# Optimization experiments

Measured on AMD Instinct MI355X. Metric: run time of the kernel, lower is better.

The kernel has to match this reference:

```python
import jax, jax.numpy as jnp
import numpy as np

N_QUBITS = 12
N_LAYERS = 4
BATCH = 4096
DIM = 2 ** N_QUBITS


def _ry(t):
    # t: (B,) real -> (B,2,2) complex64 ; RY = [[c,-s],[s,c]], c=cos(t/2), s=sin(t/2)
    c = jnp.cos(t / 2).astype(jnp.complex64)
    s = jnp.sin(t / 2).astype(jnp.complex64)
    return jnp.stack([jnp.stack([c, -s], -1), jnp.stack([s, c], -1)], -2)


def _rx(t):
    # RX = [[c,-i s],[-i s,c]]
    c = jnp.cos(t / 2).astype(jnp.complex64)
    s = (-1j) * jnp.sin(t / 2).astype(jnp.complex64)
    return jnp.stack([jnp.stack([c, s], -1), jnp.stack([s, c], -1)], -2)


def _rz(t):
    # RZ = diag(e^{-i t/2}, e^{+i t/2})
    e = jnp.exp(-0.5j * t.astype(jnp.complex64))
    z = jnp.zeros_like(e)
    return jnp.stack([jnp.stack([e, z], -1), jnp.stack([z, jnp.conj(e)], -1)], -2)


def _apply1(state, q, mat):
    # state: (B, 2^n) complex; mat: (B,2,2); qubit q is the q-th most significant bit
    B = state.shape[0]
    s = state.reshape(B, 2 ** q, 2, -1)
    return jnp.einsum('bij,bajm->baim', mat, s).reshape(B, DIM)


_CNOT_PERM = np.array([0, 1, 3, 2])  # control=1 -> flip target


def _cnot_adj(state, c):
    # CNOT(control=c, target=c+1), adjacent qubits
    B = state.shape[0]
    s = state.reshape(B, 2 ** c, 4, -1)
    return s[:, :, _CNOT_PERM, :].reshape(B, DIM)


def _parity():
    idx = np.arange(DIM)
    pop = np.zeros(DIM, dtype=np.int64)
    for k in range(N_QUBITS):
        pop += (idx >> k) & 1
    return jnp.asarray(1.0 - 2.0 * (pop % 2), dtype=jnp.float32)


def setup_inputs() -> dict:
    key = jax.random.key(0)
    k1, k2 = jax.random.split(key)
    x = jax.random.uniform(k1, (BATCH,), dtype=jnp.float32)
    thetas = jax.random.normal(k2, (N_LAYERS, N_QUBITS, 3), dtype=jnp.float32)
    return {"x": x, "thetas": thetas}


def reference(x, thetas):
    x = x.ravel()
    B = x.shape[0]
    x1 = jnp.arcsin(x)          # RY feature-map angles
    x2 = jnp.arccos(x ** 2)     # RZ feature-map angles
    state = jnp.zeros((B, DIM), jnp.complex64).at[:, 0].set(1.0)
    ry_fm = _ry(x1)
    rz_fm = _rz(x2)
    for l in range(N_LAYERS):
        for q in range(N_QUBITS):
            state = _apply1(state, q, ry_fm)
        for q in range(N_QUBITS):
            state = _apply1(state, q, rz_fm)
        for q in range(N_QUBITS):
            t = thetas[l, q]
            state = _apply1(state, q, _rx(jnp.broadcast_to(t[0], (B,))))
            state = _apply1(state, q, _rz(jnp.broadcast_to(t[1], (B,))))
            state = _apply1(state, q, _rx(jnp.broadcast_to(t[2], (B,))))
        for j in range(N_QUBITS - 1):
            state = _cnot_adj(state, j)
    abs2 = jnp.real(state) ** 2 + jnp.imag(state) ** 2
    return jnp.einsum('bs,s->b', abs2, _parity())  # <Z0 Z1 ... Z_{n-1}> per batch
```

## Files before the change

### kernel.cpp

```cpp
#include <hip/hip_runtime.h>

namespace {

constexpr int NQ = 12;
constexpr int DIM = 1 << NQ;
constexpr int THREADS = 256;

struct c32 { float r, i; };

__device__ __forceinline__ c32 cmul(c32 a, c32 b) {
    return { fmaf(a.r, b.r, -(a.i * b.i)), fmaf(a.r, b.i, a.i * b.r) };
}

__device__ __forceinline__ void bfy(c32& x, c32& y, float cb, float sb) {
    const c32 a = x, b = y;
    x.r = fmaf(cb, a.r, -(sb * b.r));
    x.i = fmaf(cb, a.i, -(sb * b.i));
    y.r = fmaf(sb, a.r, cb * b.r);
    y.i = fmaf(sb, a.i, cb * b.i);
}

template<int BP>
__device__ __forceinline__ void applyRY(c32 v[16], float cb, float sb) {
    #pragma unroll
    for (int mi = 0; mi < 8; ++mi) {
        const int i0 = ((mi >> BP) << (BP + 1)) | (mi & ((1 << BP) - 1));
        bfy(v[i0], v[i0 | (1 << BP)], cb, sb);
    }
}

__host__ __device__ constexpr int G(int t, int k) {
    for (int i = 0; i < k; ++i) t = (t ^ (t >> 1)) & 0xFFF;
    return t;
}
__host__ __device__ constexpr int Cm(int t) {
    int lo = 0;
    if (t & 0x010) lo ^= 0x2;
    if (t & 0x020) lo ^= 0x4;
    if (t & 0x040) lo ^= 0x8;
    if (t & 0x080) lo ^= 0x6;
    if (t & 0x100) lo ^= 0xA;
    if (t & 0x200) lo ^= 0xC;
    return t ^ lo;
}
__host__ __device__ constexpr int maskE_calc() {
    int m = 0;
    for (int i = 0; i < 12; ++i) {
        int v = G(Cm(1 << i), 12), p = 0;
        while (v) { p ^= (v & 1); v >>= 1; }
        if (p) m |= (1 << i);
    }
    return m;
}
constexpr int MASKE = maskE_calc();

__device__ __forceinline__ void diagTree(c32 T[16], c32 C,
                                         const c32 pf0[4], const c32 pf1[4],
                                         const c32 qv[4], int sigma) {
    const c32 one = { 1.f, 0.f };
    T[0] = C;
    #pragma unroll
    for (int m = 3; m >= 0; --m) {
        const c32 qs0 = sigma ? qv[m] : one;
        const c32 qs1 = sigma ? one : qv[m];
        const c32 g00 = cmul(pf0[m], qs0);
        const c32 g01 = cmul(pf0[m], qs1);
        const c32 g10 = cmul(pf1[m], qs0);
        const c32 g11 = cmul(pf1[m], qs1);
        #pragma unroll
        for (int e = (1 << (3 - m)) - 1; e >= 0; --e) {
            const int j0 = e << (m + 1);
            const int sfxhi = __popc(e) & 1;
            const c32 ga = sfxhi ? g01 : g00;
            const c32 gb = sfxhi ? g10 : g11;
            T[j0 | (1 << m)] = cmul(T[j0], gb);
            T[j0]            = cmul(T[j0], ga);
        }
    }
}

__global__ __launch_bounds__(THREADS)
void qcirc_kernel(const float* __restrict__ x, const float* __restrict__ thetas,
                  float* __restrict__ out) {
    __shared__ alignas(16) float2 amp[DIM];
    __shared__ float4 Vs[4 * NQ * 2];
    __shared__ float2 TbS[2][2][16];
    __shared__ float2 CHiS[2][16];
    __shared__ float2 CLoS[2][2][16];
    __shared__ float red[4];
    float4* a4 = reinterpret_cast<float4*>(amp);

    const int tid = threadIdx.x;
    const int b = blockIdx.x;

    const float xv = x[b];
    const float x1 = asinf(xv);
    const float x2 = acosf(xv * xv);
    const float cy = cosf(0.5f * x1), sy = sinf(0.5f * x1);
    const float cz = cosf(0.5f * x2), sz = sinf(0.5f * x2);
    const c32 M00 = {  cz * cy, -sz * cy };
    const c32 M01 = { -cz * sy,  sz * sy };
    const c32 M10 = {  cz * sy,  sz * sy };
    const c32 M11 = {  cz * cy,  sz * cy };

    if (tid < 4 * NQ) {
        const float* th = thetas + tid * 3;
        const float h0 = 0.5f * th[0], h1 = 0.5f * th[1], h2 = 0.5f * th[2];
        const float c0 = cosf(h0), s0 = sinf(h0);
        const float c1 = cosf(h1), s1 = sinf(h1);
        const float c2 = cosf(h2), s2 = sinf(h2);
        const c32 z0 = { c1, -s1 }, z1 = { c1, s1 };
        const c32 X00 = { c0, 0.f }, X01 = { 0.f, -s0 };
        const c32 A00 = cmul(z0, X00), A01 = cmul(z0, X01);
        const c32 A10 = cmul(z1, X01), A11 = cmul(z1, X00);
        const c32 Y00 = { c2, 0.f }, Y01 = { 0.f, -s2 };
        const c32 U00 = { Y00.r*A00.r - Y00.i*A00.i + Y01.r*A10.r - Y01.i*A10.i,
                          Y00.r*A00.i + Y00.i*A00.r + Y01.r*A10.i + Y01.i*A10.r };
        const c32 U01 = { Y00.r*A01.r - Y00.i*A01.i + Y01.r*A11.r - Y01.i*A11.i,
                          Y00.r*A01.i + Y00.i*A01.r + Y01.r*A11.i + Y01.i*A11.r };
        const c32 U10 = { Y01.r*A00.r - Y01.i*A00.i + Y00.r*A10.r - Y00.i*A10.i,
                          Y01.r*A00.i + Y01.i*A00.r + Y00.r*A10.i + Y00.i*A10.r };
        const c32 U11 = { Y01.r*A01.r - Y01.i*A01.i + Y00.r*A11.r - Y00.i*A11.i,
                          Y01.r*A01.i + Y01.i*A01.r + Y00.r*A11.i + Y00.i*A11.r };
        const c32 V00 = { U00.r*M00.r - U00.i*M00.i + U01.r*M10.r - U01.i*M10.i,
                          U00.r*M00.i + U00.i*M00.r + U01.r*M10.i + U01.i*M10.r };
        const c32 V01 = { U00.r*M01.r - U00.i*M01.i + U01.r*M11.r - U01.i*M11.i,
                          U00.r*M01.i + U00.i*M01.r + U01.r*M11.i + U01.i*M11.r };
        const c32 V10 = { U10.r*M00.r - U10.i*M00.i + U11.r*M10.r - U11.i*M10.i,
                          U10.r*M00.i + U10.i*M00.r + U11.r*M10.i + U11.i*M10.r };
        const c32 V11 = { U10.r*M01.r - U10.i*M01.i + U11.r*M11.r - U11.i*M11.i,
                          U10.r*M01.i + U10.i*M01.r + U11.r*M11.i + U11.i*M11.r };

        float cb = sqrtf(V00.r*V00.r + V00.i*V00.i);
        float sb = sqrtf(V10.r*V10.r + V10.i*V10.i);
        c32 p0, p1, q1;
        const float eps = 1e-6f;
        if (sb <= eps) {
            const float icb = 1.f / cb;
            p0 = { V00.r*icb, V00.i*icb };
            p1 = { V11.r*icb, V11.i*icb };
            q1 = { 1.f, 0.f };
            cb = 1.f; sb = 0.f;
        } else if (cb <= eps) {
            const float isb = 1.f / sb;
            p1 = { V10.r*isb, V10.i*isb };
            p0 = { -V01.r*isb, -V01.i*isb };
            q1 = { 1.f, 0.f };
            cb = 0.f; sb = 1.f;
        } else {
            const float icb = 1.f / cb, isb = 1.f / sb;
            p0 = { V00.r*icb, V00.i*icb };
            p1 = { V10.r*isb, V10.i*isb };
            const c32 t = { V11.r*p1.r + V11.i*p1.i, V11.i*p1.r - V11.r*p1.i };
            q1 = { t.r*icb, t.i*icb };
        }
        Vs[tid * 2]     = make_float4(cb, sb, p0.r, p0.i);
        Vs[tid * 2 + 1] = make_float4(p1.r, p1.i, q1.r, q1.i);
    }
    __syncthreads();

    if (tid < 64) {
        const int bK = (tid >> 5) + 1;
        const int sg = (tid >> 4) & 1;
        const int j  = tid & 15;
        c32 acc = { 1.f, 0.f };
        #pragma unroll
        for (int m = 3; m >= 0; --m) {
            const int Q = 11 - m;
            const float4 s0 = Vs[(bK*NQ+Q)*2];
            const float4 s1 = Vs[(bK*NQ+Q)*2+1];
            const float4 n1 = Vs[((bK+1)*NQ+Q)*2+1];
            const c32 pf = ((j >> m) & 1) ? c32{ s1.x, s1.y } : c32{ s0.z, s0.w };
            acc = cmul(acc, pf);
            if (sg ^ (__popc(j >> m) & 1)) acc = cmul(acc, c32{ n1.z, n1.w });
        }
        TbS[bK-1][sg][j] = make_float2(acc.r, acc.i);
    } else if (tid < 96) {
        const int idx = tid - 64;
        const int bK = (idx >> 4) + 1;
        const int h  = idx & 15;
        c32 acc = { 1.f, 0.f };
        #pragma unroll
        for (int Q = 0; Q < 4; ++Q) {
            const float4 s0 = Vs[(bK*NQ+Q)*2];
            const float4 s1 = Vs[(bK*NQ+Q)*2+1];
            const float4 n1 = Vs[((bK+1)*NQ+Q)*2+1];
            const c32 pf = ((h >> (3-Q)) & 1) ? c32{ s1.x, s1.y } : c32{ s0.z, s0.w };
            acc = cmul(acc, pf);
            if (__popc(h >> (3-Q)) & 1) acc = cmul(acc, c32{ n1.z, n1.w });
        }
        CHiS[bK-1][h] = make_float2(acc.r, acc.i);
    } else if (tid < 160) {
        const int idx = tid - 96;
        const int bK = (idx >> 5) + 1;
        const int sh = (idx >> 4) & 1;
        const int lo = idx & 15;
        c32 acc = { 1.f, 0.f };
        #pragma unroll
        for (int Q = 4; Q < 8; ++Q) {
            const float4 s0 = Vs[(bK*NQ+Q)*2];
            const float4 s1 = Vs[(bK*NQ+Q)*2+1];
            const float4 n1 = Vs[((bK+1)*NQ+Q)*2+1];
            const c32 pf = ((lo >> (7-Q)) & 1) ? c32{ s1.x, s1.y } : c32{ s0.z, s0.w };
            acc = cmul(acc, pf);
            if (sh ^ (__popc(lo >> (7-Q)) & 1)) acc = cmul(acc, c32{ n1.z, n1.w });
        }
        CLoS[bK-1][sh][lo] = make_float2(acc.r, acc.i);
    }

    {
        const int sg0 = __popc(tid) & 1;
        c32 C = { 1.f, 0.f };
        #pragma unroll
        for (int q = 0; q < 8; ++q) {
            const float4 s0 = Vs[q*2];
            const float4 s1 = Vs[q*2+1];
            const bool bit = (tid >> (7 - q)) & 1;
            const c32 e = bit ? c32{ s1.x * s0.y, s1.y * s0.y }
                             : c32{ s0.z * s0.x, s0.w * s0.x };
            C = cmul(C, e);
            const float4 n1 = Vs[(NQ+q)*2+1];
            if (__popc(tid >> (7 - q)) & 1) C = cmul(C, c32{ n1.z, n1.w });
        }
        c32 pf0[4], pf1[4], qv[4];
        #pragma unroll
        for (int m = 0; m < 4; ++m) {
            const int Q = 11 - m;
            const float4 s0 = Vs[Q*2];
            const float4 s1 = Vs[Q*2+1];
            const float4 n1 = Vs[(NQ+Q)*2+1];
            pf0[m] = { s0.z * s0.x, s0.w * s0.x };
            pf1[m] = { s1.x * s0.y, s1.y * s0.y };
            qv[m]  = { n1.z, n1.w };
        }
        c32 T[16];
        diagTree(T, C, pf0, pf1, qv, sg0);
        const int beta = Cm(tid << 4);
        #pragma unroll
        for (int m = 0; m < 8; ++m)
            a4[(beta ^ (2 * m)) >> 1] =
                make_float4(T[2*m].r, T[2*m].i, T[2*m+1].r, T[2*m+1].i);
    }
    __syncthreads();

    const int Lo = tid & 15, Hh = tid >> 4;

    #define RUN_LAYER(K)                                                            \
    {                                                                               \
                                              \
        {                                                                           \
            const float4 g0 = Vs[(K*NQ+0)*2], g1 = Vs[(K*NQ+1)*2];                  \
            const float4 g2 = Vs[(K*NQ+2)*2], g3 = Vs[(K*NQ+3)*2];                  \
            const int beta = Cm(G(tid, K));                                         \
            c32 v[16];                                                              \
            _Pragma("unroll")                                                       \
            for (int j = 0; j < 16; ++j) {                                          \
                const float2 t = amp[beta ^ Cm(G(j << 8, K))];                      \
                v[j] = { t.x, t.y };                                                \
            }                                                                       \
            applyRY<3>(v, g0.x, g0.y); applyRY<2>(v, g1.x, g1.y);                   \
            applyRY<1>(v, g2.x, g2.y); applyRY<0>(v, g3.x, g3.y);                   \
            _Pragma("unroll")                                                       \
            for (int j = 0; j < 16; ++j)                                            \
                amp[beta ^ Cm(G(j << 8, K))] = make_float2(v[j].r, v[j].i);         \
            __syncthreads();                                                        \
        }                                                                           \
                                               \
        {                                                                           \
            const float4 g0 = Vs[(K*NQ+4)*2], g1 = Vs[(K*NQ+5)*2];                  \
            const float4 g2 = Vs[(K*NQ+6)*2], g3 = Vs[(K*NQ+7)*2];                  \
            const int beta = Cm(G((Hh << 8) | Lo, K));                              \
            c32 v[16];                                                              \
            _Pragma("unroll")                                                       \
            for (int j = 0; j < 16; ++j) {                                          \
                const float2 t = amp[beta ^ Cm(G(j << 4, K))];                      \
                v[j] = { t.x, t.y };                                                \
            }                                                                       \
            applyRY<3>(v, g0.x, g0.y); applyRY<2>(v, g1.x, g1.y);                   \
            applyRY<1>(v, g2.x, g2.y); applyRY<0>(v, g3.x, g3.y);                   \
            _Pragma("unroll")                                                       \
            for (int j = 0; j < 16; ++j)                                            \
                amp[beta ^ Cm(G(j << 4, K))] = make_float2(v[j].r, v[j].i);         \
            __syncthreads();                                                        \
        }                                                                           \
            \
        {                                                                           \
            const float4 g0 = Vs[(K*NQ+8)*2],  g1 = Vs[(K*NQ+9)*2];                 \
            const float4 g2 = Vs[(K*NQ+10)*2], g3 = Vs[(K*NQ+11)*2];                \
            const int beta = Cm(G((Hh << 8) | (Lo << 4), K));                       \
            c32 v[16];                                                              \
            _Pragma("unroll")                                                       \
            for (int m = 0; m < 8; ++m) {                                           \
                const int gg = Cm(G(2 * m, K));                                     \
                const float4 F = a4[(beta ^ (gg & ~1)) >> 1];                       \
                const c32 flo = { F.x, F.y }, fhi = { F.z, F.w };                   \
                if (gg & 1) { v[2*m+1] = flo; v[2*m] = fhi; }                       \
                else        { v[2*m] = flo;   v[2*m+1] = fhi; }                     \
            }                                                                       \
            applyRY<3>(v, g0.x, g0.y); applyRY<2>(v, g1.x, g1.y);                   \
            applyRY<1>(v, g2.x, g2.y); applyRY<0>(v, g3.x, g3.y);                   \
            if constexpr (K < 3) {                                                  \
                const int sgm = __popc(tid) & 1;                                    \
                const int sgh = __popc(tid >> 4) & 1;                               \
                const float2 ch = CHiS[K-1][Hh];                                    \
                const float2 cl = CLoS[K-1][sgh][Lo];                               \
                const c32 CT = cmul(c32{ch.x,ch.y}, c32{cl.x,cl.y});                \
                _Pragma("unroll")                                                   \
                for (int j = 0; j < 16; ++j) {                                      \
                    const float2 tb = TbS[K-1][sgm][j];                             \
                    v[j] = cmul(v[j], cmul(CT, c32{tb.x, tb.y}));                   \
                }                                                                   \
            }                                                                       \
            _Pragma("unroll")                                                       \
            for (int m = 0; m < 8; ++m) {                                           \
                const int gg = Cm(G(2 * m, K));                                     \
                float4 F;                                                           \
                if (gg & 1) F = make_float4(v[2*m+1].r, v[2*m+1].i, v[2*m].r,   v[2*m].i); \
                else        F = make_float4(v[2*m].r,   v[2*m].i,   v[2*m+1].r, v[2*m+1].i); \
                a4[(beta ^ (gg & ~1)) >> 1] = F;                                    \
            }                                                                       \
            __syncthreads();                                                        \
        }                                                                           \
    }

    RUN_LAYER(1)
    RUN_LAYER(2)
    RUN_LAYER(3)
    #undef RUN_LAYER

    float acc = 0.f;
    #pragma unroll
    for (int it = 0; it < 8; ++it) {
        const int pe = (it << 9) | (tid << 1);
        const float4 F = a4[pe >> 1];
        const float m0 = fmaf(F.x, F.x, F.y * F.y);
        const float m1 = fmaf(F.z, F.z, F.w * F.w);
        acc += (__popc(pe & MASKE) & 1) ? -m0 : m0;
        acc += (__popc((pe | 1) & MASKE) & 1) ? -m1 : m1;
    }
    #pragma unroll
    for (int off = 32; off > 0; off >>= 1) acc += __shfl_down(acc, off, 64);
    if ((tid & 63) == 0) red[tid >> 6] = acc;
    __syncthreads();
    if (tid == 0) out[b] = red[0] + red[1] + red[2] + red[3];
}

}

extern "C" void kernel_launch(void* const* d_in, const int* in_sizes, int n_in,
                              void* d_out, int out_size, void* d_ws, size_t ws_size,
                              hipStream_t stream) {
    const float* x      = (const float*)d_in[0];
    const float* thetas = (const float*)d_in[1];
    float* out          = (float*)d_out;
    const int batch = in_sizes[0];
    qcirc_kernel<<<batch, THREADS, 0, stream>>>(x, thetas, out);
}
```

Before: 90.58 us.

## Replace shared-memory gate tables with per-wave register broadcasts via readlane/shuffle

Each wavefront now redundantly computes the per-qubit gate parameters and the precomputed diagonal tables (Tb, CHi, CLo) in registers and fetches them with readlane or ds_bpermute shuffles. This drops the Vs/TbS/CHiS/CLoS shared arrays and the setup __syncthreads, leaving only the amplitude buffer in LDS, and the launch bounds now request 5 blocks per SM. The intent is to cut LDS footprint and the synchronization barrier so more blocks fit per CU. The cost is redundant transcendental math in every wave, extra shuffle traffic inside the layer loops, and tighter register pressure under the occupancy bound.

```diff
diff --git a/kernel.cpp b/kernel.cpp
--- a/kernel.cpp
+++ b/kernel.cpp
@@ -10,6 +10,13 @@
 
 __device__ __forceinline__ c32 cmul(c32 a, c32 b) {
     return { fmaf(a.r, b.r, -(a.i * b.i)), fmaf(a.r, b.i, a.i * b.r) };
+}
+
+__device__ __forceinline__ float rlf(float v, int lane) {
+    return __int_as_float(__builtin_amdgcn_readlane(__float_as_int(v), lane));
+}
+__device__ __forceinline__ float shf(float v, int lane) {
+    return __shfl(v, lane, 64);
 }
 
 __device__ __forceinline__ void bfy(c32& x, c32& y, float cb, float sb) {
@@ -79,32 +86,30 @@
     }
 }
 
-__global__ __launch_bounds__(THREADS)
+__global__ __launch_bounds__(THREADS, 5)
 void qcirc_kernel(const float* __restrict__ x, const float* __restrict__ thetas,
                   float* __restrict__ out) {
     __shared__ alignas(16) float2 amp[DIM];
-    __shared__ float4 Vs[4 * NQ * 2];
-    __shared__ float2 TbS[2][2][16];
-    __shared__ float2 CHiS[2][16];
-    __shared__ float2 CLoS[2][2][16];
-    __shared__ float red[4];
     float4* a4 = reinterpret_cast<float4*>(amp);
 
     const int tid = threadIdx.x;
+    const int ln  = tid & 63;
     const int b = blockIdx.x;
 
     const float xv = x[b];
     const float x1 = asinf(xv);
     const float x2 = acosf(xv * xv);
-    const float cy = cosf(0.5f * x1), sy = sinf(0.5f * x1);
-    const float cz = cosf(0.5f * x2), sz = sinf(0.5f * x2);
-    const c32 M00 = {  cz * cy, -sz * cy };
-    const c32 M01 = { -cz * sy,  sz * sy };
-    const c32 M10 = {  cz * sy,  sz * sy };
-    const c32 M11 = {  cz * cy,  sz * cy };
-
-    if (tid < 4 * NQ) {
-        const float* th = thetas + tid * 3;
+    const float cyf = cosf(0.5f * x1), syf = sinf(0.5f * x1);
+    const float czf = cosf(0.5f * x2), szf = sinf(0.5f * x2);
+    const c32 M00 = {  czf * cyf, -szf * cyf };
+    const c32 M01 = { -czf * syf,  szf * syf };
+    const c32 M10 = {  czf * syf,  szf * syf };
+    const c32 M11 = {  czf * cyf,  szf * cyf };
+
+    float cb_, sb_, p0r, p0i, p1r, p1i, q1r, q1i;
+    {
+        const int g = ln < 48 ? ln : 0;
+        const float* th = thetas + g * 3;
         const float h0 = 0.5f * th[0], h1 = 0.5f * th[1], h2 = 0.5f * th[2];
         const float c0 = cosf(h0), s0 = sinf(h0);
         const float c1 = cosf(h1), s1 = sinf(h1);
@@ -154,58 +159,65 @@
             const c32 t = { V11.r*p1.r + V11.i*p1.i, V11.i*p1.r - V11.r*p1.i };
             q1 = { t.r*icb, t.i*icb };
         }
-        Vs[tid * 2]     = make_float4(cb, sb, p0.r, p0.i);
-        Vs[tid * 2 + 1] = make_float4(p1.r, p1.i, q1.r, q1.i);
-    }
-    __syncthreads();
-
-    if (tid < 64) {
-        const int bK = (tid >> 5) + 1;
-        const int sg = (tid >> 4) & 1;
-        const int j  = tid & 15;
+        cb_ = cb; sb_ = sb;
+        p0r = p0.r; p0i = p0.i; p1r = p1.r; p1i = p1.i; q1r = q1.r; q1i = q1.i;
+    }
+    const float a0r = p0r * cb_, a0i = p0i * cb_;
+    const float a1r = p1r * sb_, a1i = p1i * sb_;
+
+    float TbR, TbI;
+    {
+        const int K12 = 12 + ((ln >> 5) ? 12 : 0);
+        const int sg = (ln >> 4) & 1, j = ln & 15;
         c32 acc = { 1.f, 0.f };
         #pragma unroll
         for (int m = 3; m >= 0; --m) {
-            const int Q = 11 - m;
-            const float4 s0 = Vs[(bK*NQ+Q)*2];
-            const float4 s1 = Vs[(bK*NQ+Q)*2+1];
-            const float4 n1 = Vs[((bK+1)*NQ+Q)*2+1];
-            const c32 pf = ((j >> m) & 1) ? c32{ s1.x, s1.y } : c32{ s0.z, s0.w };
-            acc = cmul(acc, pf);
-            if (sg ^ (__popc(j >> m) & 1)) acc = cmul(acc, c32{ n1.z, n1.w });
-        }
-        TbS[bK-1][sg][j] = make_float2(acc.r, acc.i);
-    } else if (tid < 96) {
-        const int idx = tid - 64;
-        const int bK = (idx >> 4) + 1;
-        const int h  = idx & 15;
+            const int gl = K12 + (11 - m);
+            const float P0r = shf(p0r, gl), P0i = shf(p0i, gl);
+            const float P1r = shf(p1r, gl), P1i = shf(p1i, gl);
+            const bool bm = (j >> m) & 1;
+            acc = cmul(acc, c32{ bm ? P1r : P0r, bm ? P1i : P0i });
+            const float Qr = shf(q1r, gl + 12), Qi = shf(q1i, gl + 12);
+            const bool qc = ((sg ^ __popc(j >> m)) & 1) != 0;
+            acc = cmul(acc, c32{ qc ? Qr : 1.f, qc ? Qi : 0.f });
+        }
+        TbR = acc.r; TbI = acc.i;
+    }
+    float CHiR, CHiI;
+    {
+        const int Kh12 = 12 + (((ln >> 4) & 1) ? 12 : 0);
+        const int h = ln & 15;
         c32 acc = { 1.f, 0.f };
         #pragma unroll
         for (int Q = 0; Q < 4; ++Q) {
-            const float4 s0 = Vs[(bK*NQ+Q)*2];
-            const float4 s1 = Vs[(bK*NQ+Q)*2+1];
-            const float4 n1 = Vs[((bK+1)*NQ+Q)*2+1];
-            const c32 pf = ((h >> (3-Q)) & 1) ? c32{ s1.x, s1.y } : c32{ s0.z, s0.w };
-            acc = cmul(acc, pf);
-            if (__popc(h >> (3-Q)) & 1) acc = cmul(acc, c32{ n1.z, n1.w });
-        }
-        CHiS[bK-1][h] = make_float2(acc.r, acc.i);
-    } else if (tid < 160) {
-        const int idx = tid - 96;
-        const int bK = (idx >> 5) + 1;
-        const int sh = (idx >> 4) & 1;
-        const int lo = idx & 15;
+            const int gl = Kh12 + Q;
+            const float P0r = shf(p0r, gl), P0i = shf(p0i, gl);
+            const float P1r = shf(p1r, gl), P1i = shf(p1i, gl);
+            const bool bm = (h >> (3 - Q)) & 1;
+            acc = cmul(acc, c32{ bm ? P1r : P0r, bm ? P1i : P0i });
+            const float Qr = shf(q1r, gl + 12), Qi = shf(q1i, gl + 12);
+            const bool qc = (__popc(h >> (3 - Q)) & 1) != 0;
+            acc = cmul(acc, c32{ qc ? Qr : 1.f, qc ? Qi : 0.f });
+        }
+        CHiR = acc.r; CHiI = acc.i;
+    }
+    float CLoR, CLoI;
+    {
+        const int K12 = 12 + ((ln >> 5) ? 12 : 0);
+        const int sh = (ln >> 4) & 1, lo = ln & 15;
         c32 acc = { 1.f, 0.f };
         #pragma unroll
         for (int Q = 4; Q < 8; ++Q) {
-            const float4 s0 = Vs[(bK*NQ+Q)*2];
-            const float4 s1 = Vs[(bK*NQ+Q)*2+1];
-            const float4 n1 = Vs[((bK+1)*NQ+Q)*2+1];
-            const c32 pf = ((lo >> (7-Q)) & 1) ? c32{ s1.x, s1.y } : c32{ s0.z, s0.w };
-            acc = cmul(acc, pf);
-            if (sh ^ (__popc(lo >> (7-Q)) & 1)) acc = cmul(acc, c32{ n1.z, n1.w });
-        }
-        CLoS[bK-1][sh][lo] = make_float2(acc.r, acc.i);
+            const int gl = K12 + Q;
+            const float P0r = shf(p0r, gl), P0i = shf(p0i, gl);
+            const float P1r = shf(p1r, gl), P1i = shf(p1i, gl);
+            const bool bm = (lo >> (7 - Q)) & 1;
+            acc = cmul(acc, c32{ bm ? P1r : P0r, bm ? P1i : P0i });
+            const float Qr = shf(q1r, gl + 12), Qi = shf(q1i, gl + 12);
+            const bool qc = ((sh ^ __popc(lo >> (7 - Q))) & 1) != 0;
+            acc = cmul(acc, c32{ qc ? Qr : 1.f, qc ? Qi : 0.f });
+        }
+        CLoR = acc.r; CLoI = acc.i;
     }
 
     {
@@ -213,25 +225,21 @@
         c32 C = { 1.f, 0.f };
         #pragma unroll
         for (int q = 0; q < 8; ++q) {
-            const float4 s0 = Vs[q*2];
-            const float4 s1 = Vs[q*2+1];
+            const float E0r = rlf(a0r, q), E0i = rlf(a0i, q);
+            const float E1r = rlf(a1r, q), E1i = rlf(a1i, q);
             const bool bit = (tid >> (7 - q)) & 1;
-            const c32 e = bit ? c32{ s1.x * s0.y, s1.y * s0.y }
-                             : c32{ s0.z * s0.x, s0.w * s0.x };
-            C = cmul(C, e);
-            const float4 n1 = Vs[(NQ+q)*2+1];
-            if (__popc(tid >> (7 - q)) & 1) C = cmul(C, c32{ n1.z, n1.w });
+            C = cmul(C, c32{ bit ? E1r : E0r, bit ? E1i : E0i });
+            const float Qr = rlf(q1r, 12 + q), Qi = rlf(q1i, 12 + q);
+            const bool qb = (__popc(tid >> (7 - q)) & 1) != 0;
+            C = cmul(C, c32{ qb ? Qr : 1.f, qb ? Qi : 0.f });
         }
         c32 pf0[4], pf1[4], qv[4];
         #pragma unroll
         for (int m = 0; m < 4; ++m) {
             const int Q = 11 - m;
-            const float4 s0 = Vs[Q*2];
-            const float4 s1 = Vs[Q*2+1];
-            const float4 n1 = Vs[(NQ+Q)*2+1];
-            pf0[m] = { s0.z * s0.x, s0.w * s0.x };
-            pf1[m] = { s1.x * s0.y, s1.y * s0.y };
-            qv[m]  = { n1.z, n1.w };
+            pf0[m] = { rlf(a0r, Q), rlf(a0i, Q) };
+            pf1[m] = { rlf(a1r, Q), rlf(a1i, Q) };
+            qv[m]  = { rlf(q1r, 12 + Q), rlf(q1i, 12 + Q) };
         }
         c32 T[16];
         diagTree(T, C, pf0, pf1, qv, sg0);
@@ -249,8 +257,10 @@
     {                                                                               \
                                               \
         {                                                                           \
-            const float4 g0 = Vs[(K*NQ+0)*2], g1 = Vs[(K*NQ+1)*2];                  \
-            const float4 g2 = Vs[(K*NQ+2)*2], g3 = Vs[(K*NQ+3)*2];                  \
+            const float c0 = rlf(cb_, K*12+0), s0 = rlf(sb_, K*12+0);               \
+            const float c1 = rlf(cb_, K*12+1), s1 = rlf(sb_, K*12+1);               \
+            const float c2 = rlf(cb_, K*12+2), s2 = rlf(sb_, K*12+2);               \
+            const float c3 = rlf(cb_, K*12+3), s3 = rlf(sb_, K*12+3);               \
             const int beta = Cm(G(tid, K));                                         \
             c32 v[16];                                                              \
             _Pragma("unroll")                                                       \
@@ -258,8 +268,8 @@
                 const float2 t = amp[beta ^ Cm(G(j << 8, K))];                      \
                 v[j] = { t.x, t.y };                                                \
             }                                                                       \
-            applyRY<3>(v, g0.x, g0.y); applyRY<2>(v, g1.x, g1.y);                   \
-            applyRY<1>(v, g2.x, g2.y); applyRY<0>(v, g3.x, g3.y);                   \
+            applyRY<3>(v, c0, s0); applyRY<2>(v, c1, s1);                           \
+            applyRY<1>(v, c2, s2); applyRY<0>(v, c3, s3);                           \
             _Pragma("unroll")                                                       \
             for (int j = 0; j < 16; ++j)                                            \
                 amp[beta ^ Cm(G(j << 8, K))] = make_float2(v[j].r, v[j].i);         \
@@ -267,8 +277,10 @@
         }                                                                           \
                                                \
         {                                                                           \
-            const float4 g0 = Vs[(K*NQ+4)*2], g1 = Vs[(K*NQ+5)*2];                  \
-            const float4 g2 = Vs[(K*NQ+6)*2], g3 = Vs[(K*NQ+7)*2];                  \
+            const float c0 = rlf(cb_, K*12+4), s0 = rlf(sb_, K*12+4);               \
+            const float c1 = rlf(cb_, K*12+5), s1 = rlf(sb_, K*12+5);               \
+            const float c2 = rlf(cb_, K*12+6), s2 = rlf(sb_, K*12+6);               \
+            const float c3 = rlf(cb_, K*12+7), s3 = rlf(sb_, K*12+7);               \
             const int beta = Cm(G((Hh << 8) | Lo, K));                              \
             c32 v[16];                                                              \
             _Pragma("unroll")                                                       \
@@ -276,8 +288,8 @@
                 const float2 t = amp[beta ^ Cm(G(j << 4, K))];                      \
                 v[j] = { t.x, t.y };                                                \
             }                                                                       \
-            applyRY<3>(v, g0.x, g0.y); applyRY<2>(v, g1.x, g1.y);                   \
-            applyRY<1>(v, g2.x, g2.y); applyRY<0>(v, g3.x, g3.y);                   \
+            applyRY<3>(v, c0, s0); applyRY<2>(v, c1, s1);                           \
+            applyRY<1>(v, c2, s2); applyRY<0>(v, c3, s3);                           \
             _Pragma("unroll")                                                       \
             for (int j = 0; j < 16; ++j)                                            \
                 amp[beta ^ Cm(G(j << 4, K))] = make_float2(v[j].r, v[j].i);         \
@@ -285,8 +297,10 @@
         }                                                                           \
             \
         {                                                                           \
-            const float4 g0 = Vs[(K*NQ+8)*2],  g1 = Vs[(K*NQ+9)*2];                 \
-            const float4 g2 = Vs[(K*NQ+10)*2], g3 = Vs[(K*NQ+11)*2];                \
+            const float c0 = rlf(cb_, K*12+8),  s0 = rlf(sb_, K*12+8);              \
+            const float c1 = rlf(cb_, K*12+9),  s1 = rlf(sb_, K*12+9);              \
+            const float c2 = rlf(cb_, K*12+10), s2 = rlf(sb_, K*12+10);             \
+            const float c3 = rlf(cb_, K*12+11), s3 = rlf(sb_, K*12+11);             \
             const int beta = Cm(G((Hh << 8) | (Lo << 4), K));                       \
             c32 v[16];                                                              \
             _Pragma("unroll")                                                       \
@@ -297,18 +311,21 @@
                 if (gg & 1) { v[2*m+1] = flo; v[2*m] = fhi; }                       \
                 else        { v[2*m] = flo;   v[2*m+1] = fhi; }                     \
             }                                                                       \
-            applyRY<3>(v, g0.x, g0.y); applyRY<2>(v, g1.x, g1.y);                   \
-            applyRY<1>(v, g2.x, g2.y); applyRY<0>(v, g3.x, g3.y);                   \
+            applyRY<3>(v, c0, s0); applyRY<2>(v, c1, s1);                           \
+            applyRY<1>(v, c2, s2); applyRY<0>(v, c3, s3);                           \
             if constexpr (K < 3) {                                                  \
                 const int sgm = __popc(tid) & 1;                                    \
                 const int sgh = __popc(tid >> 4) & 1;                               \
-                const float2 ch = CHiS[K-1][Hh];                                    \
-                const float2 cl = CLoS[K-1][sgh][Lo];                               \
-                const c32 CT = cmul(c32{ch.x,ch.y}, c32{cl.x,cl.y});                \
+                const float chR = shf(CHiR, (K-1)*16 + Hh);                         \
+                const float chI = shf(CHiI, (K-1)*16 + Hh);                         \
+                const float clR = shf(CLoR, (K-1)*32 + sgh*16 + Lo);                \
+                const float clI = shf(CLoI, (K-1)*32 + sgh*16 + Lo);                \
+                const c32 CT = cmul(c32{chR, chI}, c32{clR, clI});                  \
+                const int tbb = (K-1)*32 + sgm*16;                                  \
                 _Pragma("unroll")                                                   \
                 for (int j = 0; j < 16; ++j) {                                      \
-                    const float2 tb = TbS[K-1][sgm][j];                             \
-                    v[j] = cmul(v[j], cmul(CT, c32{tb.x, tb.y}));                   \
+                    const float tr = shf(TbR, tbb + j), ti = shf(TbI, tbb + j);     \
+                    v[j] = cmul(v[j], cmul(CT, c32{tr, ti}));                       \
                 }                                                                   \
             }                                                                       \
             _Pragma("unroll")                                                       \
@@ -340,9 +357,10 @@
     }
     #pragma unroll
     for (int off = 32; off > 0; off >>= 1) acc += __shfl_down(acc, off, 64);
-    if ((tid & 63) == 0) red[tid >> 6] = acc;
     __syncthreads();
-    if (tid == 0) out[b] = red[0] + red[1] + red[2] + red[3];
+    if (ln == 0) amp[tid >> 6] = make_float2(acc, 0.f);
+    __syncthreads();
+    if (tid == 0) out[b] = amp[0].x + amp[1].x + amp[2].x + amp[3].x;
 }
 
 }
```

Measured after the change: 101.0 us. +11.5%, slower.
